# Performance work log

Hardware: AMD Instinct MI355X
Metric: run time of the kernel (lower is better)

Reference implementation:

```python
import jax, jax.numpy as jnp
import numpy as np

N = 50000      # nodes per type
E = 800000     # edges per relation
CIN = 64       # in_channels
H, O = 2, 32   # heads, out_channels
HID = H * O    # hidden
EC = 16        # edge_channels


def setup_inputs() -> dict:
    key = jax.random.key(0)
    ks = jax.random.split(key, 30)
    f = lambda i, shape, s=0.1: jax.random.normal(ks[i], shape, dtype=jnp.float32) * s
    inp = {
        'x_a': f(0, (N, CIN), 1.0), 'x_b': f(1, (N, CIN), 1.0),
        'edge_attr1': f(2, (E, EC), 1.0), 'edge_attr2': f(3, (E, EC), 1.0),
        'Wq_a': f(4, (CIN, HID)), 'Wk_a': f(5, (CIN, HID)), 'Wv_a': f(6, (CIN, HID)),
        'Wq_b': f(7, (CIN, HID)), 'Wk_b': f(8, (CIN, HID)), 'Wv_b': f(9, (CIN, HID)),
        'emb_a': f(10, (HID,)), 'emb_b': f(11, (HID,)),
        'rel1': f(12, (HID,)), 'rel2': f(13, (HID,)),
        'We': f(14, (EC, HID)), 'a_attn': f(15, (4 * O,)),
        'Wo_a': f(16, (HID, O)), 'bo_a': f(17, (O,)),
        'Wo_b': f(18, (HID, O)), 'bo_b': f(19, (O,)),
        'Wr_a': f(20, (CIN, O)), 'Wr_b': f(21, (CIN, O)),
        'row1': jax.random.randint(ks[22], (E,), 0, N),
        'col1': jax.random.randint(ks[23], (E,), 0, N),
        'row2': jax.random.randint(ks[24], (E,), 0, N),
        'col2': jax.random.randint(ks[25], (E,), 0, N),
    }
    return inp


def _edge_softmax(scores, col, num_dst):
    # softmax over incoming edges of each destination node; scores: [E, H]
    m = jax.ops.segment_max(scores, col, num_segments=num_dst)      # [N, H]
    ex = jnp.exp(scores - m[col])
    s = jax.ops.segment_sum(ex, col, num_segments=num_dst)          # [N, H]
    return ex / s[col]


def _relation(q_dst, k_src, v_src, emb_src, emb_dst, rel_emb, edge_bias,
              row, col, a_attn, num_dst):
    eb = edge_bias                                                  # [E, H, O]
    qd = q_dst[col] + emb_dst.reshape(1, H, O)
    ks = k_src[row] + emb_src.reshape(1, H, O)
    rb = jnp.broadcast_to(rel_emb.reshape(1, H, O), qd.shape)
    attn_in = jnp.concatenate([qd, ks, rb, eb], axis=-1)            # [E, H, 4O]
    scores = jnp.einsum('ehd,d->eh', jnp.tanh(attn_in), a_attn)    # [E, H]
    w = _edge_softmax(scores, col, num_dst)                         # [E, H]
    msg = v_src[row] + rel_emb.reshape(1, H, O) + eb                # [E, H, O]
    agg = jax.ops.segment_sum(msg * w[..., None], col, num_segments=num_dst)
    return agg.reshape(num_dst, H * O)


def reference(x_a, x_b, edge_attr1, edge_attr2,
              Wq_a, Wk_a, Wv_a, Wq_b, Wk_b, Wv_b,
              emb_a, emb_b, rel1, rel2, We, a_attn,
              Wo_a, bo_a, Wo_b, bo_b, Wr_a, Wr_b,
              row1, col1, row2, col2):
    q_a = (x_a @ Wq_a).reshape(-1, H, O)
    k_a = (x_a @ Wk_a).reshape(-1, H, O)
    v_a = (x_a @ Wv_a).reshape(-1, H, O)
    q_b = (x_b @ Wq_b).reshape(-1, H, O)
    k_b = (x_b @ Wk_b).reshape(-1, H, O)
    v_b = (x_b @ Wv_b).reshape(-1, H, O)

    # relation r1: a -> b
    eb1 = (edge_attr1 @ We).reshape(-1, H, O)
    out_b = _relation(q_b, k_a, v_a, emb_a, emb_b, rel1, eb1, row1, col1, a_attn, N)
    # relation r2: b -> a
    eb2 = (edge_attr2 @ We).reshape(-1, H, O)
    out_a = _relation(q_a, k_b, v_b, emb_b, emb_a, rel2, eb2, row2, col2, a_attn, N)

    fin_a = out_a @ Wo_a + bo_a + x_a @ Wr_a                        # [N, O]
    fin_b = out_b @ Wo_b + bo_b + x_b @ Wr_b                        # [N, O]
    return jnp.concatenate([fin_a, fin_b], axis=0)                  # [2N, O]
```

## Files before the change

### kernel.cpp

```cpp
#include <hip/hip_runtime.h>
#include <hip/hip_bf16.h>

typedef __hip_bfloat16 bf16;
typedef __attribute__((ext_vector_type(8))) short short8;
typedef __attribute__((ext_vector_type(4))) float float4v;

static __device__ __forceinline__ float b2f(bf16 x) { return __bfloat162float(x); }

static __device__ __forceinline__ float ldf(const void* p, size_t i, int f32) {
    return f32 ? ((const float*)p)[i] : b2f(((const bf16*)p)[i]);
}
static __device__ __forceinline__ void stf(void* p, size_t i, int f32, float v) {
    if (f32) ((float*)p)[i] = v;
    else     ((bf16*)p)[i] = __float2bfloat16(v);
}
static __device__ __forceinline__ unsigned short f2bf_bits(float f) {
    bf16 h = __float2bfloat16(f);
    return *(unsigned short*)&h;
}

static __device__ __forceinline__ float fast_tanh(float x) {
    float t = __expf(2.f * x);
    return 1.f - 2.f * __builtin_amdgcn_rcpf(t + 1.f);
}

__global__ void detect_kernel(const unsigned short* __restrict__ a, int* __restrict__ flag)
{
    __shared__ int cnt;
    if (threadIdx.x == 0) cnt = 0;
    __syncthreads();
    unsigned e = (a[threadIdx.x] >> 7) & 0xFF;
    if (e < 100 || e > 133) atomicAdd(&cnt, 1);
    __syncthreads();
    if (threadIdx.x == 0) *flag = (cnt >= 16) ? 1 : 0;
}

__global__ __launch_bounds__(256) void prep_small_kernel(
    const void* __restrict__ W0, const void* __restrict__ W1,
    const void* __restrict__ W2, const void* __restrict__ W3,
    const void* __restrict__ W4, const void* __restrict__ W5,
    const void* __restrict__ Wr_a, const void* __restrict__ Wr_b,
    const void* __restrict__ We,
    const void* __restrict__ Wo_a, const void* __restrict__ Wo_b,
    const void* __restrict__ rel1, const void* __restrict__ rel2,
    const void* __restrict__ a_attn, const int* __restrict__ flagp,
    unsigned short* __restrict__ wt,
    float* __restrict__ M1, float* __restrict__ c321,
    float* __restrict__ M2, float* __restrict__ c322,
    float* __restrict__ cvals)
{
    const int f32 = *flagp;
    const int bid = blockIdx.x;
    if (bid < 6) {
        const void* src;
        switch (bid) {
            case 0: src = W0; break; case 1: src = W1; break; case 2: src = W2; break;
            case 3: src = W3; break; case 4: src = W4; break; default: src = W5; break;
        }
        unsigned short* dst = wt + bid * 4096;
        for (int i = threadIdx.x; i < 4096; i += 256) {
            int c = i >> 6, j = i & 63;
            dst[j * 64 + c] = f2bf_bits(ldf(src, c * 64 + j, f32));
        }
    } else if (bid < 8) {
        const void* src = (bid == 6) ? Wr_a : Wr_b;
        unsigned short* dst = wt + 24576 + (bid - 6) * 2048;
        for (int i = threadIdx.x; i < 2048; i += 256) {
            int c = i >> 5, j = i & 31;
            dst[j * 64 + c] = f2bf_bits(ldf(src, c * 32 + j, f32));
        }
    } else if (bid < 10) {
        const int sel = bid - 8;
        const void* Wo  = sel ? Wo_a : Wo_b;
        const void* rel = sel ? rel2 : rel1;
        float* M   = sel ? M2 : M1;
        float* c32 = sel ? c322 : c321;
        const int t = threadIdx.x;
        for (int i = t; i < 1024; i += 256) {
            int m = i >> 5, j = i & 31;
            int h = m >> 4, c = m & 15;
            float s = 0.f;
            for (int jj = 0; jj < 32; ++jj)
                s += ldf(We, c * 64 + h * 32 + jj, f32) * ldf(Wo, (size_t)(h * 32 + jj) * 32 + j, f32);
            M[m * 32 + j] = s;
        }
        if (t < 32) {
            float s2 = 0.f;
            for (int ch = 0; ch < 64; ++ch)
                s2 += ldf(rel, ch, f32) * ldf(Wo, (size_t)ch * 32 + t, f32);
            c32[t] = s2;
        }
        if (t == 252 || t == 253) {
            int h = t - 252;
            float s3 = 0.f;
            for (int l = 0; l < 32; ++l)
                s3 += tanhf(ldf(rel, h * 32 + l, f32)) * ldf(a_attn, 64 + l, f32);
            cvals[sel * 2 + h] = s3;
        }
    } else {
        unsigned short* wet = wt + 28672;
        for (int i = threadIdx.x; i < 1024; i += 256) {
            int n = i >> 4, k = i & 15;
            wet[n * 16 + k] = f2bf_bits(ldf(We, k * 64 + n, f32));
        }
    }
}

__global__ __launch_bounds__(256) void node_prep_mfma_kernel(
    const void* __restrict__ x_a, const void* __restrict__ x_b,
    const unsigned short* __restrict__ wt,
    const void* __restrict__ emb_a, const void* __restrict__ emb_b,
    const void* __restrict__ a_attn, const int* __restrict__ flagp,
    unsigned short* __restrict__ v_a, unsigned short* __restrict__ v_b,
    float* __restrict__ r_a, float* __restrict__ r_b,
    float* __restrict__ sq_a, float* __restrict__ sk_a,
    float* __restrict__ sq_b, float* __restrict__ sk_b,
    const int* __restrict__ col1, const int* __restrict__ col2,
    int* __restrict__ cnt,
    int n_nodes, int tiles, int mfma_blocks, int num_e)
{
    const int f32 = *flagp;

    if ((int)blockIdx.x >= mfma_blocks) {
        const int hb  = blockIdx.x - mfma_blocks;
        const int sel = hb & 1;
        const int bx  = hb >> 1;
        const int* col = sel ? col2 : col1;
        const int rb = sel ? n_nodes : 0;
        int e = bx * 256 + threadIdx.x;
        if (e < num_e) atomicAdd(&cnt[rb + col[e]], 1);
        return;
    }

    const int wave_id = blockIdx.x * 4 + (threadIdx.x >> 6);
    if (wave_id >= 2 * tiles) return;
    const int type = (wave_id >= tiles);
    const int tile = type ? (wave_id - tiles) : wave_id;

    const void* xp = type ? x_b : x_a;
    const unsigned short* wq = wt + (type ? 3 * 4096 : 0);
    const unsigned short* wk = wq + 4096;
    const unsigned short* wv = wk + 4096;
    const unsigned short* wr = wt + 24576 + (type ? 2048 : 0);
    const void* embp = type ? emb_b : emb_a;
    unsigned short* v_out = type ? v_b : v_a;
    float*  r_out  = type ? r_b : r_a;
    float2* sq_out = (float2*)(type ? sq_b : sq_a);
    float2* sk_out = (float2*)(type ? sk_b : sk_a);

    const int lane = threadIdx.x & 63;
    const int ml   = lane & 15;
    const int g    = lane >> 4;
    const int g8   = g * 8;

    float embc[4], acq[4], ack[4];
    #pragma unroll
    for (int t = 0; t < 4; ++t) {
        int colt = t * 16 + ml;
        embc[t] = ldf(embp, colt, f32);
        acq[t]  = ldf(a_attn, colt & 31, f32);
        ack[t]  = ldf(a_attn, 32 + (colt & 31), f32);
    }

    short8 Bq[4][2], Bk[4][2], Bv[4][2], Br[2][2];
    #pragma unroll
    for (int t = 0; t < 4; ++t) {
        const int rowo = (t * 16 + ml) * 64;
        #pragma unroll
        for (int kh = 0; kh < 2; ++kh) {
            const int o = rowo + kh * 32 + g8;
            Bq[t][kh] = __builtin_bit_cast(short8, *(const uint4*)(wq + o));
            Bk[t][kh] = __builtin_bit_cast(short8, *(const uint4*)(wk + o));
            Bv[t][kh] = __builtin_bit_cast(short8, *(const uint4*)(wv + o));
            if (t < 2)
                Br[t][kh] = __builtin_bit_cast(short8, *(const uint4*)(wr + o));
        }
    }

    const int n0 = tile << 4;
    int nr = n0 + ml; if (nr > n_nodes - 1) nr = n_nodes - 1;
    short8 A0, A1;
    if (f32) {
        const float4* xr = (const float4*)((const float*)xp + (size_t)nr * 64);
        float4 f0 = xr[2*g], f1 = xr[2*g+1], f2 = xr[8+2*g], f3 = xr[9+2*g];
        short8 a0, a1;
        a0[0]=(short)f2bf_bits(f0.x); a0[1]=(short)f2bf_bits(f0.y);
        a0[2]=(short)f2bf_bits(f0.z); a0[3]=(short)f2bf_bits(f0.w);
        a0[4]=(short)f2bf_bits(f1.x); a0[5]=(short)f2bf_bits(f1.y);
        a0[6]=(short)f2bf_bits(f1.z); a0[7]=(short)f2bf_bits(f1.w);
        a1[0]=(short)f2bf_bits(f2.x); a1[1]=(short)f2bf_bits(f2.y);
        a1[2]=(short)f2bf_bits(f2.z); a1[3]=(short)f2bf_bits(f2.w);
        a1[4]=(short)f2bf_bits(f3.x); a1[5]=(short)f2bf_bits(f3.y);
        a1[6]=(short)f2bf_bits(f3.z); a1[7]=(short)f2bf_bits(f3.w);
        A0 = a0; A1 = a1;
    } else {
        const uint4* xr = (const uint4*)((const bf16*)xp + (size_t)nr * 64);
        A0 = __builtin_bit_cast(short8, xr[g]);
        A1 = __builtin_bit_cast(short8, xr[4 + g]);
    }

    float4v accq[4], acck[4], accv[4], accr[2];
    #pragma unroll
    for (int t = 0; t < 4; ++t) {
        float4v z = {0.f, 0.f, 0.f, 0.f};
        accq[t] = z; acck[t] = z; accv[t] = z;
        if (t < 2) accr[t] = z;
    }
    #pragma unroll
    for (int t = 0; t < 4; ++t) {
        accq[t] = __builtin_amdgcn_mfma_f32_16x16x32_bf16(A0, Bq[t][0], accq[t], 0, 0, 0);
        accq[t] = __builtin_amdgcn_mfma_f32_16x16x32_bf16(A1, Bq[t][1], accq[t], 0, 0, 0);
        acck[t] = __builtin_amdgcn_mfma_f32_16x16x32_bf16(A0, Bk[t][0], acck[t], 0, 0, 0);
        acck[t] = __builtin_amdgcn_mfma_f32_16x16x32_bf16(A1, Bk[t][1], acck[t], 0, 0, 0);
        accv[t] = __builtin_amdgcn_mfma_f32_16x16x32_bf16(A0, Bv[t][0], accv[t], 0, 0, 0);
        accv[t] = __builtin_amdgcn_mfma_f32_16x16x32_bf16(A1, Bv[t][1], accv[t], 0, 0, 0);
        if (t < 2) {
            accr[t] = __builtin_amdgcn_mfma_f32_16x16x32_bf16(A0, Br[t][0], accr[t], 0, 0, 0);
            accr[t] = __builtin_amdgcn_mfma_f32_16x16x32_bf16(A1, Br[t][1], accr[t], 0, 0, 0);
        }
    }

    #pragma unroll
    for (int t = 0; t < 4; ++t) {
        #pragma unroll
        for (int r = 0; r < 4; ++r) {
            int node = n0 + g * 4 + r;
            if (node < n_nodes) {
                v_out[(size_t)node * 64 + t * 16 + ml] = f2bf_bits(accv[t][r]);
                if (t < 2) r_out[(size_t)node * 32 + t * 16 + ml] = accr[t][r];
            }
        }
    }

    #pragma unroll
    for (int r = 0; r < 4; ++r) {
        float q0 = fast_tanh(accq[0][r] + embc[0]) * acq[0]
                 + fast_tanh(accq[1][r] + embc[1]) * acq[1];
        float q1 = fast_tanh(accq[2][r] + embc[2]) * acq[2]
                 + fast_tanh(accq[3][r] + embc[3]) * acq[3];
        float k0 = fast_tanh(acck[0][r] + embc[0]) * ack[0]
                 + fast_tanh(acck[1][r] + embc[1]) * ack[1];
        float k1 = fast_tanh(acck[2][r] + embc[2]) * ack[2]
                 + fast_tanh(acck[3][r] + embc[3]) * ack[3];
        #pragma unroll
        for (int o = 1; o < 16; o <<= 1) {
            q0 += __shfl_xor(q0, o, 64); q1 += __shfl_xor(q1, o, 64);
            k0 += __shfl_xor(k0, o, 64); k1 += __shfl_xor(k1, o, 64);
        }
        int node = n0 + g * 4 + r;
        if (ml == 0 && node < n_nodes) {
            sq_out[node] = make_float2(q0, q1);
            sk_out[node] = make_float2(k0, k1);
        }
    }
}

__global__ __launch_bounds__(256) void scan1_kernel(const int* __restrict__ cnt,
                                                    int* __restrict__ partial, int n)
{
    __shared__ int wsum[4];
    int t = threadIdx.x;
    int i0 = blockIdx.x * 512 + 2 * t;
    int s = ((i0 < n) ? cnt[i0] : 0) + ((i0 + 1 < n) ? cnt[i0 + 1] : 0);
    #pragma unroll
    for (int o = 32; o; o >>= 1) s += __shfl_xor(s, o, 64);
    if ((t & 63) == 0) wsum[t >> 6] = s;
    __syncthreads();
    if (t == 0) partial[blockIdx.x] = wsum[0] + wsum[1] + wsum[2] + wsum[3];
}

__global__ void scan2_kernel(const int* __restrict__ partial, int* __restrict__ pp,
                             int* __restrict__ off, int nch, int noff)
{
    int lane = threadIdx.x;
    int running = 0;
    for (int base = 0; base < nch; base += 64) {
        int i = base + lane;
        int o = (i < nch) ? partial[i] : 0;
        int v = o;
        #pragma unroll
        for (int d = 1; d < 64; d <<= 1) {
            int u = __shfl_up(v, d, 64);
            if (lane >= d) v += u;
        }
        if (i < nch) pp[i] = running + v - o;
        running += __shfl(v, 63, 64);
    }
    if (lane == 0) off[noff] = running;
}

__global__ __launch_bounds__(256) void scan3_kernel(const int* __restrict__ cnt,
                                                    const int* __restrict__ pp,
                                                    int* __restrict__ off,
                                                    int* __restrict__ cursor, int n)
{
    __shared__ int tmp[256];
    int t = threadIdx.x;
    int i0 = blockIdx.x * 512 + 2 * t;
    int v0 = (i0 < n) ? cnt[i0] : 0;
    int v1 = (i0 + 1 < n) ? cnt[i0 + 1] : 0;
    int pair = v0 + v1;
    tmp[t] = pair;
    __syncthreads();
    for (int d = 1; d < 256; d <<= 1) {
        int x = (t >= d) ? tmp[t - d] : 0;
        __syncthreads();
        tmp[t] += x;
        __syncthreads();
    }
    int excl = tmp[t] - pair + pp[blockIdx.x];
    if (i0 < n)     { off[i0] = excl;          cursor[i0] = excl; }
    if (i0 + 1 < n) { off[i0 + 1] = excl + v0; cursor[i0 + 1] = excl + v0; }
}

__global__ __launch_bounds__(256) void edge_score_scatter_kernel(
    const void* __restrict__ ea1p, const void* __restrict__ ea2p,
    const unsigned short* __restrict__ wet,
    const int* __restrict__ row1, const int* __restrict__ col1,
    const int* __restrict__ row2, const int* __restrict__ col2,
    const float* __restrict__ sq_bp, const float* __restrict__ sk_ap,
    const float* __restrict__ sq_ap, const float* __restrict__ sk_bp,
    const float* __restrict__ cvals, const void* __restrict__ a_attn,
    const int* __restrict__ flagp, int* __restrict__ cursor,
    uint4* __restrict__ payload, int n_nodes, int num_e)
{
    const int f32 = *flagp;
    const int sel = blockIdx.x & 1;
    const int bx  = blockIdx.x >> 1;
    const void* ea = sel ? ea2p : ea1p;
    const int* row = sel ? row2 : row1;
    const int* col = sel ? col2 : col1;
    const float* sq_dst = sel ? sq_ap : sq_bp;
    const float* sk_src = sel ? sk_bp : sk_ap;
    const int rb = sel ? n_nodes : 0;

    const int lane = threadIdx.x & 63;
    const int wv   = threadIdx.x >> 6;
    const int ml   = lane & 15;
    const int g    = lane >> 4;
    const int rsel = lane & 3;

    const int base = bx * 256 + wv * 64;
    if (base >= num_e) return;

    const short8 zero8 = {0, 0, 0, 0, 0, 0, 0, 0};

    short8 B[4];
    #pragma unroll
    for (int t = 0; t < 4; ++t)
        B[t] = (g < 2) ? __builtin_bit_cast(short8, *(const uint4*)(wet + (t * 16 + ml) * 16 + g * 8))
                       : zero8;
    float av[4];
    #pragma unroll
    for (int t = 0; t < 4; ++t) av[t] = ldf(a_attn, 96 + ((t * 16 + ml) & 31), f32);
    const float c0 = cvals[sel * 2 + 0];
    const float c1 = cvals[sel * 2 + 1];

    short8 A[4];
    #pragma unroll
    for (int it = 0; it < 4; ++it) {
        int ec = base + it * 16 + ml; if (ec > num_e - 1) ec = num_e - 1;
        if (g < 2) {
            if (f32) {
                const float4* p = (const float4*)((const float*)ea + (size_t)ec * 16 + g * 8);
                float4 f0 = p[0], f1 = p[1];
                short8 a;
                a[0] = (short)f2bf_bits(f0.x); a[1] = (short)f2bf_bits(f0.y);
                a[2] = (short)f2bf_bits(f0.z); a[3] = (short)f2bf_bits(f0.w);
                a[4] = (short)f2bf_bits(f1.x); a[5] = (short)f2bf_bits(f1.y);
                a[6] = (short)f2bf_bits(f1.z); a[7] = (short)f2bf_bits(f1.w);
                A[it] = a;
            } else {
                A[it] = __builtin_bit_cast(short8, *(const uint4*)((const bf16*)ea + (size_t)ec * 16 + g * 8));
            }
        } else {
            A[it] = zero8;
        }
    }

    int ppos[4]; unsigned psrc[4]; float2 psq[4], psk[4];
    #pragma unroll
    for (int it = 0; it < 4; ++it) {
        ppos[it] = 0; psrc[it] = 0;
        psq[it] = make_float2(0.f, 0.f); psk[it] = make_float2(0.f, 0.f);
    }
    if (ml < 4) {
        int pcol[4];
        #pragma unroll
        for (int it = 0; it < 4; ++it) {
            int e = base + it * 16 + g * 4 + rsel;
            int ec = (e < num_e) ? e : (num_e - 1);
            pcol[it] = col[ec];
            psrc[it] = (unsigned)row[ec];
        }
        #pragma unroll
        for (int it = 0; it < 4; ++it) {
            psq[it] = ((const float2*)sq_dst)[pcol[it]];
            psk[it] = ((const float2*)sk_src)[psrc[it]];
        }
        #pragma unroll
        for (int it = 0; it < 4; ++it) {
            int e = base + it * 16 + g * 4 + rsel;
            ppos[it] = (e < num_e) ? atomicAdd(&cursor[rb + pcol[it]], 1) : 0;
        }
    }

    #pragma unroll
    for (int it = 0; it < 4; ++it) {
        const int e0 = base + it * 16;
        if (e0 < num_e) {
            float4v z = {0.f, 0.f, 0.f, 0.f};
            float4v acc0 = z, acc1 = z, acc2 = z, acc3 = z;
            acc0 = __builtin_amdgcn_mfma_f32_16x16x32_bf16(A[it], B[0], acc0, 0, 0, 0);
            acc1 = __builtin_amdgcn_mfma_f32_16x16x32_bf16(A[it], B[1], acc1, 0, 0, 0);
            acc2 = __builtin_amdgcn_mfma_f32_16x16x32_bf16(A[it], B[2], acc2, 0, 0, 0);
            acc3 = __builtin_amdgcn_mfma_f32_16x16x32_bf16(A[it], B[3], acc3, 0, 0, 0);

            float s0[4], s1[4];
            #pragma unroll
            for (int r = 0; r < 4; ++r) {
                s0[r] = fast_tanh(acc0[r]) * av[0] + fast_tanh(acc1[r]) * av[1];
                s1[r] = fast_tanh(acc2[r]) * av[2] + fast_tanh(acc3[r]) * av[3];
            }
            #pragma unroll
            for (int o = 1; o < 16; o <<= 1) {
                #pragma unroll
                for (int r = 0; r < 4; ++r) {
                    s0[r] += __shfl_xor(s0[r], o, 64);
                    s1[r] += __shfl_xor(s1[r], o, 64);
                }
            }

            const bool fin = (ml < 4) && (e0 + g * 4 + rsel < num_e);
            if (fin) {
                float a0 = (rsel == 0) ? s0[0] : (rsel == 1) ? s0[1] : (rsel == 2) ? s0[2] : s0[3];
                float a1 = (rsel == 0) ? s1[0] : (rsel == 1) ? s1[1] : (rsel == 2) ? s1[2] : s1[3];
                float v0 = fminf(30.f, fmaxf(-30.f, a0 + psq[it].x + psk[it].x + c0));
                float v1 = fminf(30.f, fmaxf(-30.f, a1 + psq[it].y + psk[it].y + c1));
                uint4* rec = payload + (size_t)3 * ppos[it];
                rec[0] = make_uint4(psrc[it], __float_as_uint(__expf(v0)),
                                    __float_as_uint(__expf(v1)), 0u);
            }
            const int srcl = ((lane & 12) << 2) | (lane & 3);
            const int posx = __shfl(ppos[it], srcl, 64);
            if (lane < 32 && (e0 + ml < num_e)) {
                uint4* rec = payload + (size_t)3 * posx;
                rec[1 + g] = __builtin_bit_cast(uint4, A[it]);
            }
        }
    }
}

__global__ __launch_bounds__(256) void agg_final_kernel(
    const uint4* __restrict__ payload, const int* __restrict__ off,
    const unsigned short* __restrict__ v_a, const unsigned short* __restrict__ v_b,
    const float* __restrict__ r_a, const float* __restrict__ r_b,
    const void* __restrict__ Wo_a, const void* __restrict__ Wo_b,
    const void* __restrict__ bo_a, const void* __restrict__ bo_b,
    const float* __restrict__ M1, const float* __restrict__ M2,
    const float* __restrict__ c321, const float* __restrict__ c322,
    const int* __restrict__ flagp, void* __restrict__ out,
    int n_nodes, int nbh)
{
    const int sel = blockIdx.x & 1;
    const int bx  = blockIdx.x >> 1;
    const unsigned short* v_src = sel ? v_b : v_a;
    const float* r_src = sel ? r_a : r_b;
    const void*  Wo    = sel ? Wo_a : Wo_b;
    const void*  bo    = sel ? bo_a : bo_b;
    const float* M     = sel ? M2 : M1;
    const float* c32   = sel ? c322 : c321;
    const int relbase  = sel ? n_nodes : 0;
    const size_t out_off = sel ? 0 : (size_t)n_nodes * 32;

    const int f32  = *flagp;
    const int lane = threadIdx.x & 63;
    const int wv   = threadIdx.x >> 6;
    const int j    = lane & 31;
    const int half = lane >> 5;
    const int c16  = lane & 15;
    const bool hi  = (lane >= 32);

    __shared__ float stage[4][96];

    float WoR[32], MR[16];
    const int cb = half * 32;
    #pragma unroll
    for (int cc = 0; cc < 32; ++cc)
        WoR[cc] = ldf(Wo, (size_t)(cb + cc) * 32 + j, f32);
    const int ub = half * 16;
    #pragma unroll
    for (int cc = 0; cc < 16; ++cc) MR[cc] = M[(ub + cc) * 32 + j];
    const float boR  = ldf(bo, j, f32);
    const float c32R = c32[j];

    const int stride = nbh * 4;
    const int iters  = (n_nodes + stride - 1) / stride;
    int d = bx * 4 + wv;

    int dd0 = (d < n_nodes) ? d : (n_nodes - 1);
    int b_c  = off[relbase + dd0];
    int en_c = off[relbase + dd0 + 1];
    float rv_c = r_src[(size_t)dd0 * 32 + j];

    for (int it = 0; it < iters; ++it, d += stride) {
        const bool valid = (d < n_nodes);
        const int dd  = valid ? d : (n_nodes - 1);

        int b_n = 0, en_n = 0; float rv_n = 0.f;
        if (it + 1 < iters) {
            int dn  = d + stride;
            int ddn = (dn < n_nodes) ? dn : (n_nodes - 1);
            b_n  = off[relbase + ddn];
            en_n = off[relbase + ddn + 1];
            rv_n = r_src[(size_t)ddn * 32 + j];
        }

        const int b   = __builtin_amdgcn_readfirstlane(b_c);
        const int en  = __builtin_amdgcn_readfirstlane(en_c);
        const int deg = en - b;
        const float rv = rv_c;

        float den0 = 0.f, den1 = 0.f, y = 0.f, ua = 0.f;
        int k = b;
        #pragma unroll 1
        for (; k + 8 <= en; k += 8) {
            uint4 m[8];
            #pragma unroll
            for (int q = 0; q < 8; ++q) m[q] = payload[(size_t)3 * (k + q)];
            float ev[8];
            #pragma unroll
            for (int q = 0; q < 8; ++q) {
                const unsigned short* pq = (const unsigned short*)(payload + (size_t)3 * (k + q) + 1);
                ev[q] = __uint_as_float((unsigned)pq[c16] << 16);
            }
            float vv[8];
            #pragma unroll
            for (int q = 0; q < 8; ++q)
                vv[q] = __uint_as_float((unsigned)v_src[(size_t)m[q].x * 64 + lane] << 16);
            #pragma unroll
            for (int q = 0; q < 8; ++q) {
                float e0 = __uint_as_float(m[q].y), e1 = __uint_as_float(m[q].z);
                den0 += e0; den1 += e1;
                float xw = hi ? e1 : e0;
                y  = fmaf(xw, vv[q], y);
                ua = fmaf(xw, ev[q], ua);
            }
        }
        #pragma unroll 1
        for (; k < en; ++k) {
            uint4 mm = payload[(size_t)3 * k];
            const unsigned short* pq = (const unsigned short*)(payload + (size_t)3 * k + 1);
            float evs = __uint_as_float((unsigned)pq[c16] << 16);
            float vvs = __uint_as_float((unsigned)v_src[(size_t)mm.x * 64 + lane] << 16);
            float e0 = __uint_as_float(mm.y), e1 = __uint_as_float(mm.z);
            den0 += e0; den1 += e1;
            float xw = hi ? e1 : e0;
            y  = fmaf(xw, vvs, y);
            ua = fmaf(xw, evs, ua);
        }

        float inv0 = (deg > 0) ? __builtin_amdgcn_rcpf(den0) : 0.f;
        float inv1 = (deg > 0) ? __builtin_amdgcn_rcpf(den1) : 0.f;
        const float invh = hi ? inv1 : inv0;
        y  *= invh;
        ua *= invh;

        float* st = stage[wv];
        st[lane] = y;
        if ((lane & 31) < 16) st[64 + half * 16 + c16] = ua;
        __asm__ volatile("s_waitcnt lgkmcnt(0)" ::: "memory");

        float acc = 0.f;
        #pragma unroll
        for (int cc = 0; cc < 32; ++cc)
            acc = fmaf(st[cb + cc], WoR[cc], acc);
        #pragma unroll
        for (int cc = 0; cc < 16; ++cc)
            acc = fmaf(st[64 + ub + cc], MR[cc], acc);

        float other = __shfl(acc, lane ^ 32, 64);
        if (valid && lane < 32) {
            float o = acc + other + boR + rv + ((deg > 0) ? c32R : 0.f);
            stf(out, out_off + (size_t)dd * 32 + j, f32, o);
        }
        __asm__ volatile("" ::: "memory");
        __builtin_amdgcn_wave_barrier();

        b_c = b_n; en_c = en_n; rv_c = rv_n;
    }
}

extern "C" void kernel_launch(void* const* d_in, const int* in_sizes, int n_in,
                              void* d_out, int out_size, void* d_ws, size_t ws_size,
                              hipStream_t stream)
{
    const void* x_a   = d_in[0];
    const void* x_b   = d_in[1];
    const void* ea1   = d_in[2];
    const void* ea2   = d_in[3];
    const void* Wq_a  = d_in[4];
    const void* Wk_a  = d_in[5];
    const void* Wv_a  = d_in[6];
    const void* Wq_b  = d_in[7];
    const void* Wk_b  = d_in[8];
    const void* Wv_b  = d_in[9];
    const void* emb_a = d_in[10];
    const void* emb_b = d_in[11];
    const void* rel1  = d_in[12];
    const void* rel2  = d_in[13];
    const void* We    = d_in[14];
    const void* a_at  = d_in[15];
    const void* Wo_a  = d_in[16];
    const void* bo_a  = d_in[17];
    const void* Wo_b  = d_in[18];
    const void* bo_b  = d_in[19];
    const void* Wr_a  = d_in[20];
    const void* Wr_b  = d_in[21];
    const int*  row1  = (const int*)d_in[22];
    const int*  col1  = (const int*)d_in[23];
    const int*  row2  = (const int*)d_in[24];
    const int*  col2  = (const int*)d_in[25];

    const int N = in_sizes[0] / 64;
    const int E = in_sizes[22];

    float* ws = (float*)d_ws;
    size_t off = 0;
    int*   flag = (int*)ws;        off += 64;
    unsigned short* v_a = (unsigned short*)(ws + off); off += (size_t)N * 32;
    unsigned short* v_b = (unsigned short*)(ws + off); off += (size_t)N * 32;
    float* r_a  = ws + off;        off += (size_t)N * 32;
    float* r_b  = ws + off;        off += (size_t)N * 32;
    float* sq_a = ws + off;        off += (size_t)N * 2;
    float* sk_a = ws + off;        off += (size_t)N * 2;
    float* sq_b = ws + off;        off += (size_t)N * 2;
    float* sk_b = ws + off;        off += (size_t)N * 2;
    float* cvals = ws + off;       off += 4;
    off = (off + 3) & ~(size_t)3;
    unsigned short* wt = (unsigned short*)(ws + off); off += 29696 / 2;
    float* M1   = ws + off;        off += 1024;
    float* c321 = ws + off;        off += 32;
    float* M2   = ws + off;        off += 1024;
    float* c322 = ws + off;        off += 32;
    int*   cnt    = (int*)(ws + off);  off += (size_t)2 * N;
    int*   offs   = (int*)(ws + off);  off += (size_t)2 * N + 2;
    int*   cursor = (int*)(ws + off);  off += (size_t)2 * N;
    int*   partial = (int*)(ws + off); off += 512;
    int*   pp      = (int*)(ws + off); off += 512;
    off = (off + 3) & ~(size_t)3;
    uint4* payload = (uint4*)(ws + off); off += (size_t)2 * E * 12;

    const int tiles        = (N + 15) >> 4;
    const int mfma_blocks  = (2 * tiles + 3) / 4;
    const int eb_blocks    = (E + 255) / 256;
    const int score_blocks = (E + 255) / 256;
    const int nch          = (2 * N + 511) / 512;
    const int agg_half     = 2048;

    detect_kernel<<<1, 128, 0, stream>>>((const unsigned short*)a_at, flag);
    hipMemsetAsync(cnt, 0, (size_t)2 * N * sizeof(int), stream);

    prep_small_kernel<<<11, 256, 0, stream>>>(
        Wq_a, Wk_a, Wv_a, Wq_b, Wk_b, Wv_b, Wr_a, Wr_b,
        We, Wo_a, Wo_b, rel1, rel2, a_at, flag,
        wt, M1, c321, M2, c322, cvals);

    node_prep_mfma_kernel<<<mfma_blocks + 2 * eb_blocks, 256, 0, stream>>>(
        x_a, x_b, wt, emb_a, emb_b, a_at, flag,
        v_a, v_b, r_a, r_b, sq_a, sk_a, sq_b, sk_b,
        col1, col2, cnt, N, tiles, mfma_blocks, E);

    scan1_kernel<<<nch, 256, 0, stream>>>(cnt, partial, 2 * N);
    scan2_kernel<<<1, 64, 0, stream>>>(partial, pp, offs, nch, 2 * N);
    scan3_kernel<<<nch, 256, 0, stream>>>(cnt, pp, offs, cursor, 2 * N);

    edge_score_scatter_kernel<<<2 * score_blocks, 256, 0, stream>>>(
        ea1, ea2, wt + 28672, row1, col1, row2, col2,
        sq_b, sk_a, sq_a, sk_b, cvals, a_at, flag,
        cursor, payload, N, E);

    agg_final_kernel<<<2 * agg_half, 256, 0, stream>>>(
        payload, offs, v_a, v_b, r_a, r_b, Wo_a, Wo_b, bo_a, bo_b,
        M1, M2, c321, c322, flag, d_out, N, agg_half);
}
```

Baseline: 525.3 us.

## Reuse histogram atomic ranks for scatter positions, drop cursor atomics

The counting pass now stores the value returned by each edge's atomicAdd as that edge's rank within its destination bucket. The scatter kernel computes each payload slot as offs[col] + rank instead of running a second atomicAdd on a cursor array, and scan3 no longer writes cursor. This removes a full round of contended global atomics in exchange for writing and reading an extra rank array of 2E ints. The aggregation grid size is also doubled.

```diff
diff --git a/kernel.cpp b/kernel.cpp
--- a/kernel.cpp
+++ b/kernel.cpp
@@ -116,7 +116,7 @@
     float* __restrict__ sq_a, float* __restrict__ sk_a,
     float* __restrict__ sq_b, float* __restrict__ sk_b,
     const int* __restrict__ col1, const int* __restrict__ col2,
-    int* __restrict__ cnt,
+    int* __restrict__ cnt, int* __restrict__ rank_out,
     int n_nodes, int tiles, int mfma_blocks, int num_e)
 {
     const int f32 = *flagp;
@@ -128,7 +128,8 @@
         const int* col = sel ? col2 : col1;
         const int rb = sel ? n_nodes : 0;
         int e = bx * 256 + threadIdx.x;
-        if (e < num_e) atomicAdd(&cnt[rb + col[e]], 1);
+        if (e < num_e)
+            rank_out[(size_t)sel * num_e + e] = atomicAdd(&cnt[rb + col[e]], 1);
         return;
     }
 
@@ -291,8 +292,7 @@
 
 __global__ __launch_bounds__(256) void scan3_kernel(const int* __restrict__ cnt,
                                                     const int* __restrict__ pp,
-                                                    int* __restrict__ off,
-                                                    int* __restrict__ cursor, int n)
+                                                    int* __restrict__ off, int n)
 {
     __shared__ int tmp[256];
     int t = threadIdx.x;
@@ -309,8 +309,8 @@
         __syncthreads();
     }
     int excl = tmp[t] - pair + pp[blockIdx.x];
-    if (i0 < n)     { off[i0] = excl;          cursor[i0] = excl; }
-    if (i0 + 1 < n) { off[i0 + 1] = excl + v0; cursor[i0 + 1] = excl + v0; }
+    if (i0 < n)     off[i0] = excl;
+    if (i0 + 1 < n) off[i0 + 1] = excl + v0;
 }
 
 __global__ __launch_bounds__(256) void edge_score_scatter_kernel(
@@ -321,7 +321,8 @@
     const float* __restrict__ sq_bp, const float* __restrict__ sk_ap,
     const float* __restrict__ sq_ap, const float* __restrict__ sk_bp,
     const float* __restrict__ cvals, const void* __restrict__ a_attn,
-    const int* __restrict__ flagp, int* __restrict__ cursor,
+    const int* __restrict__ flagp,
+    const int* __restrict__ offs, const int* __restrict__ rankp,
     uint4* __restrict__ payload, int n_nodes, int num_e)
 {
     const int f32 = *flagp;
@@ -333,6 +334,7 @@
     const float* sq_dst = sel ? sq_ap : sq_bp;
     const float* sk_src = sel ? sk_bp : sk_ap;
     const int rb = sel ? n_nodes : 0;
+    const int* rankr = rankp + (size_t)sel * num_e;
 
     const int lane = threadIdx.x & 63;
     const int wv   = threadIdx.x >> 6;
@@ -355,6 +357,20 @@
     for (int t = 0; t < 4; ++t) av[t] = ldf(a_attn, 96 + ((t * 16 + ml) & 31), f32);
     const float c0 = cvals[sel * 2 + 0];
     const float c1 = cvals[sel * 2 + 1];
+
+    int pcol[4]; unsigned psrc[4]; int prank[4];
+    #pragma unroll
+    for (int it = 0; it < 4; ++it) { pcol[it] = 0; psrc[it] = 0; prank[it] = 0; }
+    if (ml < 4) {
+        #pragma unroll
+        for (int it = 0; it < 4; ++it) {
+            int e = base + it * 16 + g * 4 + rsel;
+            int ec = (e < num_e) ? e : (num_e - 1);
+            pcol[it]  = col[ec];
+            psrc[it]  = (unsigned)row[ec];
+            prank[it] = rankr[ec];
+        }
+    }
 
     short8 A[4];
     #pragma unroll
@@ -378,30 +394,18 @@
         }
     }
 
-    int ppos[4]; unsigned psrc[4]; float2 psq[4], psk[4];
+    int ppos[4]; float2 psq[4], psk[4];
     #pragma unroll
     for (int it = 0; it < 4; ++it) {
-        ppos[it] = 0; psrc[it] = 0;
+        ppos[it] = 0;
         psq[it] = make_float2(0.f, 0.f); psk[it] = make_float2(0.f, 0.f);
     }
     if (ml < 4) {
-        int pcol[4];
-        #pragma unroll
-        for (int it = 0; it < 4; ++it) {
-            int e = base + it * 16 + g * 4 + rsel;
-            int ec = (e < num_e) ? e : (num_e - 1);
-            pcol[it] = col[ec];
-            psrc[it] = (unsigned)row[ec];
-        }
         #pragma unroll
         for (int it = 0; it < 4; ++it) {
             psq[it] = ((const float2*)sq_dst)[pcol[it]];
             psk[it] = ((const float2*)sk_src)[psrc[it]];
-        }
-        #pragma unroll
-        for (int it = 0; it < 4; ++it) {
-            int e = base + it * 16 + g * 4 + rsel;
-            ppos[it] = (e < num_e) ? atomicAdd(&cursor[rb + pcol[it]], 1) : 0;
+            ppos[it] = offs[rb + pcol[it]] + prank[it];
         }
     }
 
@@ -645,7 +649,7 @@
     float* c322 = ws + off;        off += 32;
     int*   cnt    = (int*)(ws + off);  off += (size_t)2 * N;
     int*   offs   = (int*)(ws + off);  off += (size_t)2 * N + 2;
-    int*   cursor = (int*)(ws + off);  off += (size_t)2 * N;
+    int*   rankp  = (int*)(ws + off);  off += (size_t)2 * E;
     int*   partial = (int*)(ws + off); off += 512;
     int*   pp      = (int*)(ws + off); off += 512;
     off = (off + 3) & ~(size_t)3;
@@ -656,7 +660,7 @@
     const int eb_blocks    = (E + 255) / 256;
     const int score_blocks = (E + 255) / 256;
     const int nch          = (2 * N + 511) / 512;
-    const int agg_half     = 2048;
+    const int agg_half     = 4096;
 
     detect_kernel<<<1, 128, 0, stream>>>((const unsigned short*)a_at, flag);
     hipMemsetAsync(cnt, 0, (size_t)2 * N * sizeof(int), stream);
@@ -669,16 +673,16 @@
     node_prep_mfma_kernel<<<mfma_blocks + 2 * eb_blocks, 256, 0, stream>>>(
         x_a, x_b, wt, emb_a, emb_b, a_at, flag,
         v_a, v_b, r_a, r_b, sq_a, sk_a, sq_b, sk_b,
-        col1, col2, cnt, N, tiles, mfma_blocks, E);
+        col1, col2, cnt, rankp, N, tiles, mfma_blocks, E);
 
     scan1_kernel<<<nch, 256, 0, stream>>>(cnt, partial, 2 * N);
     scan2_kernel<<<1, 64, 0, stream>>>(partial, pp, offs, nch, 2 * N);
-    scan3_kernel<<<nch, 256, 0, stream>>>(cnt, pp, offs, cursor, 2 * N);
+    scan3_kernel<<<nch, 256, 0, stream>>>(cnt, pp, offs, 2 * N);
 
     edge_score_scatter_kernel<<<2 * score_blocks, 256, 0, stream>>>(
         ea1, ea2, wt + 28672, row1, col1, row2, col2,
         sq_b, sk_a, sq_a, sk_b, cvals, a_at, flag,
-        cursor, payload, N, E);
+        offs, rankp, payload, N, E);
 
     agg_final_kernel<<<2 * agg_half, 256, 0, stream>>>(
         payload, offs, v_a, v_b, r_a, r_b, Wo_a, Wo_b, bo_a, bo_b,
```

Measured after the change: 525.3 us. About the same (-0.0%).
